# Kernel tuning notes

Measured on AMD Instinct MI355X. Metric: run time of the kernel, lower is better.

The kernel has to match this reference:

```python
import jax, jax.numpy as jnp
import numpy as np
import math

B, T = 32768, 34
VOCAB = 14
SQRT_HD = math.sqrt(3.0)

def _pos_flat_index():
    # flatten (source, index) pairs into indices of a [14,3] table:
    # rows 0-9 = digit spiral enc, row 10 = z10_enc, rows 11-13 = special_enc
    flat = []
    for p in range(34):
        if p < 10:
            flat.append(p)
        elif p == 10:
            flat.append(11 + 0)
        elif p < 21:
            flat.append(p - 11)
        elif p == 21:
            flat.append(11 + 1)
        elif p < 33:
            z = p - 22
            flat.append(z if z < 10 else 10)
        else:
            flat.append(11 + 2)
    return np.array(flat, dtype=np.int32)

POS_FLAT = _pos_flat_index()

def setup_inputs() -> dict:
    key = jax.random.key(0)
    ks = jax.random.split(key, 12)
    r = lambda k, s: jax.random.normal(k, s, dtype=jnp.float32)
    return {
        'idx': jax.random.randint(ks[0], (B, T), 0, VOCAB, dtype=jnp.int64),
        'tok_emb': r(ks[1], (14, 3)),
        'pos_params': r(ks[2], (4,)),
        'z10_enc': r(ks[3], (1, 3)),
        'special_enc': r(ks[4], (3, 3)),
        'wq': r(ks[5], (3, 6)), 'wk': r(ks[6], (3, 6)), 'wv': r(ks[7], (3, 6)),
        'wo': r(ks[8], (6, 6)),
        'ln1_g': jnp.ones(6), 'ln1_b': jnp.zeros(6),
        'ln2_g': jnp.ones(6), 'ln2_b': jnp.zeros(6),
        'lnf_g': jnp.ones(6), 'lnf_b': jnp.zeros(6),
        'ffn_w1': r(ks[9], (6, 2)), 'ffn_b1': jnp.zeros(2),
        'ffn_w2': r(ks[10], (2, 6)), 'ffn_b2': jnp.zeros(6),
        'head_w': r(ks[11], (6, 3)),
    }

def _ln(x, g, b):
    mu = x.mean(-1, keepdims=True)
    var = ((x - mu) ** 2).mean(-1, keepdims=True)
    return (x - mu) * jax.lax.rsqrt(var + 1e-5) * g + b

def _forward(idx, tok_emb, pos_params, z10_enc, special_enc, wq, wk, wv, wo,
             ln1_g, ln1_b, ln2_g, ln2_b, lnf_g, lnf_b,
             ffn_w1, ffn_b1, ffn_w2, ffn_b2, head_w):
    amp, phase, slope, offset = pos_params[0], pos_params[1], pos_params[2], pos_params[3]
    i = jnp.arange(10, dtype=jnp.float32)
    ang = 2.0 * math.pi * i / 10.0 + phase
    digit = jnp.stack([amp * jnp.cos(ang), amp * jnp.sin(ang), slope * i + offset], -1)  # [10,3]
    table = jnp.concatenate([digit, z10_enc, special_enc], 0)  # [14,3]
    Tn = idx.shape[1]
    pos = table[POS_FLAT][:Tn]  # [T,3]
    tok = tok_emb[idx]  # [B,T,3]
    x = jnp.concatenate([tok, jnp.broadcast_to(pos, tok.shape)], -1)  # [B,T,6]
    h = _ln(x, ln1_g, ln1_b)
    h_tok, h_pos = h[..., :3], h[..., 3:]
    Bn = idx.shape[0]
    q = (h_pos @ wq).reshape(Bn, Tn, 2, 3)
    k = (h_pos @ wk).reshape(Bn, Tn, 2, 3)
    v = (h_tok @ wv).reshape(Bn, Tn, 2, 3)
    attn = jnp.einsum('bqhd,bkhd->bhqk', q, k) / SQRT_HD
    mask = jnp.tril(jnp.ones((Tn, Tn), bool))
    attn = jax.nn.softmax(jnp.where(mask, attn, -jnp.inf), axis=-1)
    o = jnp.einsum('bhqk,bkhd->bqhd', attn, v).reshape(Bn, Tn, 6)
    x = x + o @ wo
    h2 = _ln(x, ln2_g, ln2_b)
    x = x + (jax.nn.gelu(h2 @ ffn_w1 + ffn_b1, approximate=False) @ ffn_w2 + ffn_b2)
    x = _ln(x, lnf_g, lnf_b)
    return (x @ head_w) @ tok_emb.T  # [B,T,14]

def reference(idx, tok_emb, pos_params, z10_enc, special_enc, wq, wk, wv, wo,
              ln1_g, ln1_b, ln2_g, ln2_b, lnf_g, lnf_b,
              ffn_w1, ffn_b1, ffn_w2, ffn_b2, head_w):
    return _forward(idx, tok_emb, pos_params, z10_enc, special_enc, wq, wk, wv, wo,
                    ln1_g, ln1_b, ln2_g, ln2_b, lnf_g, lnf_b,
                    ffn_w1, ffn_b1, ffn_w2, ffn_b2, head_w)
```

## Files before the change

kernel.cpp:

```cpp
#include <hip/hip_runtime.h>
#include <math.h>

#define BT    34
#define TPR   17
#define RPB   15
#define BLOCK 256

typedef float v2f __attribute__((ext_vector_type(2)));
typedef float v4f __attribute__((ext_vector_type(4)));

#define QSCALE 0.83294037332470f

#if __has_builtin(__builtin_amdgcn_exp2f)
#define EXP2(x) __builtin_amdgcn_exp2f(x)
#else
#define EXP2(x) exp2f(x)
#endif

__device__ __forceinline__ void ln6p(const v2f* x, const float* g, const float* b, v2f* o) {
  v2f mu = (x[0]+x[1]+x[2]+x[3]+x[4]+x[5]) * (1.0f/6.0f);
  v2f v = (v2f){0.f, 0.f};
  #pragma unroll
  for (int c = 0; c < 6; ++c) { v2f d = x[c]-mu; v += d*d; }
  v2f inv = (v2f){ rsqrtf(v.x*(1.0f/6.0f) + 1e-5f),
                   rsqrtf(v.y*(1.0f/6.0f) + 1e-5f) };
  #pragma unroll
  for (int c = 0; c < 6; ++c) o[c] = (x[c]-mu)*inv*g[c] + b[c];
}

__global__ __launch_bounds__(BLOCK, 5)
void addtrans_kernel(const int* __restrict__ idx,
                     const float* __restrict__ tok_emb,
                     const float* __restrict__ pos_params,
                     const float* __restrict__ z10_enc,
                     const float* __restrict__ special_enc,
                     const float* __restrict__ wq,
                     const float* __restrict__ wk,
                     const float* __restrict__ wv,
                     const float* __restrict__ wo,
                     const float* __restrict__ ln1_g, const float* __restrict__ ln1_b,
                     const float* __restrict__ ln2_g, const float* __restrict__ ln2_b,
                     const float* __restrict__ lnf_g, const float* __restrict__ lnf_b,
                     const float* __restrict__ ffn_w1, const float* __restrict__ ffn_b1,
                     const float* __restrict__ ffn_w2, const float* __restrict__ ffn_b2,
                     const float* __restrict__ head_w,
                     float* __restrict__ out, int B)
{
  __shared__ __align__(16) float s_mem[RPB*BT*14];
  __shared__ int   s_idx[RPB*BT];
  __shared__ float s_te[42];
  __shared__ float s_pos[BT*3];
  __shared__ float s_wq[18], s_wk[18], s_wv[18], s_wo[36], s_hw[18];
  __shared__ float s_g1[6], s_b1[6], s_g2[6], s_b2[6], s_gf[6], s_bf[6];
  __shared__ float s_w1[12], s_w2[12], s_fb1[2], s_fb2[6];

  const int tid = threadIdx.x;
  const int b0  = blockIdx.x * RPB;

  if (tid < 42) s_te[tid] = tok_emb[tid];
  if (tid < 18) { s_wq[tid]=wq[tid]; s_wk[tid]=wk[tid]; s_wv[tid]=wv[tid]; s_hw[tid]=head_w[tid]; }
  if (tid < 36) s_wo[tid] = wo[tid];
  if (tid < 12) { s_w1[tid]=ffn_w1[tid]; s_w2[tid]=ffn_w2[tid]; }
  if (tid < 6)  { s_g1[tid]=ln1_g[tid]; s_b1[tid]=ln1_b[tid];
                  s_g2[tid]=ln2_g[tid]; s_b2[tid]=ln2_b[tid];
                  s_gf[tid]=lnf_g[tid]; s_bf[tid]=lnf_b[tid];
                  s_fb2[tid]=ffn_b2[tid]; }
  if (tid < 2)  s_fb1[tid] = ffn_b1[tid];
  {
    int nr = B - b0; if (nr > RPB) nr = RPB;
    const int tot = nr * BT;
    for (int i = tid; i < tot; i += BLOCK) s_idx[i] = idx[b0*BT + i];
  }
  if (tid < BT) {
    int p = tid, f;
    if (p < 10) f = p;
    else if (p == 10) f = 11;
    else if (p < 21) f = p - 11;
    else if (p == 21) f = 12;
    else if (p < 33) { int z = p - 22; f = (z < 10) ? z : 10; }
    else f = 13;
    float e0, e1, e2;
    if (f < 10) {
      float amp = pos_params[0], ph = pos_params[1], sl = pos_params[2], of = pos_params[3];
      float ang = 0.62831853071795864769f * (float)f + ph;
      e0 = amp * cosf(ang); e1 = amp * sinf(ang); e2 = sl * (float)f + of;
    } else if (f == 10) { e0 = z10_enc[0]; e1 = z10_enc[1]; e2 = z10_enc[2]; }
    else { int u = f - 11; e0 = special_enc[u*3]; e1 = special_enc[u*3+1]; e2 = special_enc[u*3+2]; }
    s_pos[tid*3+0] = e0; s_pos[tid*3+1] = e1; s_pos[tid*3+2] = e2;
  }
  __syncthreads();

  const int row = tid % RPB;
  const int j   = tid / RPB;
  const int b   = b0 + row;
  const bool active = (j < TPR) && (b < B);

  v2f qpA[3], qpB[3];
  v2f x6[6];

  if (active) {
    const int tA = j, tB = j + TPR;
    const int vA = s_idx[row*BT + tA];
    const int vB = s_idx[row*BT + tB];
    #pragma unroll
    for (int c = 0; c < 3; ++c) {
      x6[c]   = (v2f){ s_te[vA*3+c],  s_te[vB*3+c]  };
      x6[3+c] = (v2f){ s_pos[tA*3+c], s_pos[tB*3+c] };
    }
    v2f h[6];
    ln6p(x6, s_g1, s_b1, h);
    v2f q6[6], k6[6], v6[6];
    #pragma unroll
    for (int c = 0; c < 6; ++c) {
      q6[c] = h[3]*s_wq[c] + h[4]*s_wq[6+c] + h[5]*s_wq[12+c];
      k6[c] = h[3]*s_wk[c] + h[4]*s_wk[6+c] + h[5]*s_wk[12+c];
      v6[c] = h[0]*s_wv[c] + h[1]*s_wv[6+c] + h[2]*s_wv[12+c];
    }
    #pragma unroll
    for (int d = 0; d < 3; ++d) {
      qpA[d] = (v2f){ q6[d].x, q6[3+d].x } * QSCALE;
      qpB[d] = (v2f){ q6[d].y, q6[3+d].y } * QSCALE;
    }
    v4f* pA = (v4f*)&s_mem[(tA*RPB + row)*12];
    pA[0] = (v4f){ k6[0].x, k6[3].x, k6[1].x, k6[4].x };
    pA[1] = (v4f){ k6[2].x, k6[5].x, v6[0].x, v6[3].x };
    pA[2] = (v4f){ v6[1].x, v6[4].x, v6[2].x, v6[5].x };
    v4f* pB = (v4f*)&s_mem[(tB*RPB + row)*12];
    pB[0] = (v4f){ k6[0].y, k6[3].y, k6[1].y, k6[4].y };
    pB[1] = (v4f){ k6[2].y, k6[5].y, v6[0].y, v6[3].y };
    pB[2] = (v4f){ v6[1].y, v6[4].y, v6[2].y, v6[5].y };
  }
  __syncthreads();

  v2f l0 = (v2f){0.f,0.f}, l1 = (v2f){0.f,0.f};
  v2f o0[3] = {(v2f){0.f,0.f},(v2f){0.f,0.f},(v2f){0.f,0.f}};
  v2f o1[3] = {(v2f){0.f,0.f},(v2f){0.f,0.f},(v2f){0.f,0.f}};
  if (active) {
    const float* kvbase = s_mem + row*12;
    v4f A  = ((const v4f*)kvbase)[0];
    v4f Bv = ((const v4f*)kvbase)[1];
    v4f C  = ((const v4f*)kvbase)[2];
    for (int k = 0; k <= j; ++k) {
      const v4f Ac = A, Bc = Bv, Cc = C;
      const v4f* nxt = (const v4f*)(kvbase + (k+1)*(RPB*12));
      A = nxt[0]; Bv = nxt[1]; C = nxt[2];
      v2f kA = (v2f){Ac.x, Ac.y}, kB = (v2f){Ac.z, Ac.w}, kC = (v2f){Bc.x, Bc.y};
      v2f vA = (v2f){Bc.z, Bc.w}, vB = (v2f){Cc.x, Cc.y}, vC = (v2f){Cc.z, Cc.w};
      v2f s0 = qpA[0]*kA + qpA[1]*kB + qpA[2]*kC;
      v2f p0 = (v2f){EXP2(s0.x), EXP2(s0.y)};
      l0 += p0; o0[0] += p0*vA; o0[1] += p0*vB; o0[2] += p0*vC;
      v2f s1 = qpB[0]*kA + qpB[1]*kB + qpB[2]*kC;
      v2f p1 = (v2f){EXP2(s1.x), EXP2(s1.y)};
      l1 += p1; o1[0] += p1*vA; o1[1] += p1*vB; o1[2] += p1*vC;
    }
    for (int i = 1; i <= TPR; ++i) {
      const int k = j + i;
      const v4f Ac = A, Bc = Bv, Cc = C;
      const v4f* nxt = (const v4f*)(kvbase + (k+1)*(RPB*12));
      A = nxt[0]; Bv = nxt[1]; C = nxt[2];
      v2f kA = (v2f){Ac.x, Ac.y}, kB = (v2f){Ac.z, Ac.w}, kC = (v2f){Bc.x, Bc.y};
      v2f vA = (v2f){Bc.z, Bc.w}, vB = (v2f){Cc.x, Cc.y}, vC = (v2f){Cc.z, Cc.w};
      v2f s1 = qpB[0]*kA + qpB[1]*kB + qpB[2]*kC;
      v2f p1 = (v2f){EXP2(s1.x), EXP2(s1.y)};
      l1 += p1; o1[0] += p1*vA; o1[1] += p1*vB; o1[2] += p1*vC;
    }
  }
  __syncthreads();

  if (active) {
    const float rA0 = __builtin_amdgcn_rcpf(l0.x);
    const float rA1 = __builtin_amdgcn_rcpf(l0.y);
    const float rB0 = __builtin_amdgcn_rcpf(l1.x);
    const float rB1 = __builtin_amdgcn_rcpf(l1.y);
    v2f a6[6];
    a6[0] = (v2f){ o0[0].x*rA0, o1[0].x*rB0 };
    a6[1] = (v2f){ o0[1].x*rA0, o1[1].x*rB0 };
    a6[2] = (v2f){ o0[2].x*rA0, o1[2].x*rB0 };
    a6[3] = (v2f){ o0[0].y*rA1, o1[0].y*rB1 };
    a6[4] = (v2f){ o0[1].y*rA1, o1[1].y*rB1 };
    a6[5] = (v2f){ o0[2].y*rA1, o1[2].y*rB1 };
    v2f xn[6];
    #pragma unroll
    for (int c = 0; c < 6; ++c) {
      xn[c] = x6[c]
            + a6[0]*s_wo[c]    + a6[1]*s_wo[6+c]  + a6[2]*s_wo[12+c]
            + a6[3]*s_wo[18+c] + a6[4]*s_wo[24+c] + a6[5]*s_wo[30+c];
    }
    v2f h2[6];
    ln6p(xn, s_g2, s_b2, h2);
    v2f a0 = (v2f){s_fb1[0], s_fb1[0]};
    v2f a1 = (v2f){s_fb1[1], s_fb1[1]};
    #pragma unroll
    for (int d = 0; d < 6; ++d) { a0 += h2[d]*s_w1[d*2]; a1 += h2[d]*s_w1[d*2+1]; }
    const float KIS2 = 0.70710678118654752440f;
    v2f g0 = (v2f){ 0.5f*a0.x*(1.0f + erff(a0.x*KIS2)),
                    0.5f*a0.y*(1.0f + erff(a0.y*KIS2)) };
    v2f g1 = (v2f){ 0.5f*a1.x*(1.0f + erff(a1.x*KIS2)),
                    0.5f*a1.y*(1.0f + erff(a1.y*KIS2)) };
    #pragma unroll
    for (int c = 0; c < 6; ++c) xn[c] += g0*s_w2[c] + g1*s_w2[6+c] + s_fb2[c];
    v2f xf[6];
    ln6p(xn, s_gf, s_bf, xf);
    v2f y0 = (v2f){0.f,0.f}, y1 = (v2f){0.f,0.f}, y2 = (v2f){0.f,0.f};
    #pragma unroll
    for (int c = 0; c < 6; ++c) {
      y0 += xf[c]*s_hw[c*3+0]; y1 += xf[c]*s_hw[c*3+1]; y2 += xf[c]*s_hw[c*3+2];
    }
    v2f* lpA = (v2f*)&s_mem[(row*BT + j      )*14];
    v2f* lpB = (v2f*)&s_mem[(row*BT + j + TPR)*14];
    #pragma unroll
    for (int u = 0; u < 7; ++u) {
      const int c0 = 2*u, c1 = 2*u+1;
      v2f lg0 = y0*s_te[c0*3+0] + y1*s_te[c0*3+1] + y2*s_te[c0*3+2];
      v2f lg1 = y0*s_te[c1*3+0] + y1*s_te[c1*3+1] + y2*s_te[c1*3+2];
      lpA[u] = (v2f){ lg0.x, lg1.x };
      lpB[u] = (v2f){ lg0.y, lg1.y };
    }
  }
  __syncthreads();

  {
    int nrows = B - b0; if (nrows > RPB) nrows = RPB;
    if (nrows > 0) {
      const int n4 = nrows * (BT*14/4);
      v4f* dst = reinterpret_cast<v4f*>(out + (size_t)b0 * (BT*14));
      const v4f* src = reinterpret_cast<const v4f*>(s_mem);
      for (int i = tid; i < n4; i += BLOCK)
        __builtin_nontemporal_store(src[i], dst + i);
    }
  }
}

extern "C" void kernel_launch(void* const* d_in, const int* in_sizes, int n_in,
                              void* d_out, int out_size, void* d_ws, size_t ws_size,
                              hipStream_t stream) {
  const int B = in_sizes[0] / BT;
  const int grid = (B + RPB - 1) / RPB;
  addtrans_kernel<<<grid, BLOCK, 0, stream>>>(
      (const int*)d_in[0],   (const float*)d_in[1], (const float*)d_in[2],
      (const float*)d_in[3], (const float*)d_in[4], (const float*)d_in[5],
      (const float*)d_in[6], (const float*)d_in[7], (const float*)d_in[8],
      (const float*)d_in[9], (const float*)d_in[10], (const float*)d_in[11],
      (const float*)d_in[12], (const float*)d_in[13], (const float*)d_in[14],
      (const float*)d_in[15], (const float*)d_in[16], (const float*)d_in[17],
      (const float*)d_in[18], (const float*)d_in[19],
      (float*)d_out, B);
}
```

Measured before the change: 133.6 us.

## Fold LayerNorm affine into weights and write logits directly to global memory

Folds the LayerNorm gamma and beta into the following projection weights and biases, so each LayerNorm only normalises. The shared-memory output staging and its trailing barriers are removed: logits go straight to global memory as 8-byte stores, and idx is read directly from global instead of through shared memory. Shared memory shrinks, so the launch bound is raised to 6 blocks per SIMD, and the second attention loop gets unroll 4. The direct stores are strided per thread rather than coalesced 16-byte nontemporal writes, which risks poorer write efficiency on this output-bound kernel.

Result: slower. 140.5 us (+5.2%).

```diff
diff --git a/kernel.cpp b/kernel.cpp
--- a/kernel.cpp
+++ b/kernel.cpp
@@ -17,7 +17,7 @@
 #define EXP2(x) exp2f(x)
 #endif
 
-__device__ __forceinline__ void ln6p(const v2f* x, const float* g, const float* b, v2f* o) {
+__device__ __forceinline__ void ln6n(const v2f* x, v2f* o) {
   v2f mu = (x[0]+x[1]+x[2]+x[3]+x[4]+x[5]) * (1.0f/6.0f);
   v2f v = (v2f){0.f, 0.f};
   #pragma unroll
@@ -25,10 +25,10 @@
   v2f inv = (v2f){ rsqrtf(v.x*(1.0f/6.0f) + 1e-5f),
                    rsqrtf(v.y*(1.0f/6.0f) + 1e-5f) };
   #pragma unroll
-  for (int c = 0; c < 6; ++c) o[c] = (x[c]-mu)*inv*g[c] + b[c];
+  for (int c = 0; c < 6; ++c) o[c] = (x[c]-mu)*inv;
 }
 
-__global__ __launch_bounds__(BLOCK, 5)
+__global__ __launch_bounds__(BLOCK, 6)
 void addtrans_kernel(const int* __restrict__ idx,
                      const float* __restrict__ tok_emb,
                      const float* __restrict__ pos_params,
@@ -46,30 +46,46 @@
                      const float* __restrict__ head_w,
                      float* __restrict__ out, int B)
 {
-  __shared__ __align__(16) float s_mem[RPB*BT*14];
-  __shared__ int   s_idx[RPB*BT];
+  __shared__ __align__(16) float s_mem[RPB*BT*12 + 180];
   __shared__ float s_te[42];
   __shared__ float s_pos[BT*3];
-  __shared__ float s_wq[18], s_wk[18], s_wv[18], s_wo[36], s_hw[18];
-  __shared__ float s_g1[6], s_b1[6], s_g2[6], s_b2[6], s_gf[6], s_bf[6];
-  __shared__ float s_w1[12], s_w2[12], s_fb1[2], s_fb2[6];
+  __shared__ float s_wqf[18], s_wkf[18], s_wvf[18];
+  __shared__ float s_qb[6], s_kb[6], s_vb[6];
+  __shared__ float s_wo[36];
+  __shared__ float s_w1f[12], s_fb1f[2];
+  __shared__ float s_w2[12], s_fb2[6];
+  __shared__ float s_hwf[18], s_yb[3];
 
   const int tid = threadIdx.x;
   const int b0  = blockIdx.x * RPB;
 
   if (tid < 42) s_te[tid] = tok_emb[tid];
-  if (tid < 18) { s_wq[tid]=wq[tid]; s_wk[tid]=wk[tid]; s_wv[tid]=wv[tid]; s_hw[tid]=head_w[tid]; }
+  if (tid < 18) {
+    const int r = tid / 6;
+    s_wqf[tid] = wq[tid] * ln1_g[3+r];
+    s_wkf[tid] = wk[tid] * ln1_g[3+r];
+    s_wvf[tid] = wv[tid] * ln1_g[r];
+    s_hwf[tid] = head_w[tid] * lnf_g[tid/3];
+  }
   if (tid < 36) s_wo[tid] = wo[tid];
-  if (tid < 12) { s_w1[tid]=ffn_w1[tid]; s_w2[tid]=ffn_w2[tid]; }
-  if (tid < 6)  { s_g1[tid]=ln1_g[tid]; s_b1[tid]=ln1_b[tid];
-                  s_g2[tid]=ln2_g[tid]; s_b2[tid]=ln2_b[tid];
-                  s_gf[tid]=lnf_g[tid]; s_bf[tid]=lnf_b[tid];
-                  s_fb2[tid]=ffn_b2[tid]; }
-  if (tid < 2)  s_fb1[tid] = ffn_b1[tid];
-  {
-    int nr = B - b0; if (nr > RPB) nr = RPB;
-    const int tot = nr * BT;
-    for (int i = tid; i < tot; i += BLOCK) s_idx[i] = idx[b0*BT + i];
+  if (tid < 12) { s_w1f[tid] = ffn_w1[tid] * ln2_g[tid>>1]; s_w2[tid] = ffn_w2[tid]; }
+  if (tid < 6)  {
+    s_qb[tid] = ln1_b[3]*wq[tid] + ln1_b[4]*wq[6+tid] + ln1_b[5]*wq[12+tid];
+    s_kb[tid] = ln1_b[3]*wk[tid] + ln1_b[4]*wk[6+tid] + ln1_b[5]*wk[12+tid];
+    s_vb[tid] = ln1_b[0]*wv[tid] + ln1_b[1]*wv[6+tid] + ln1_b[2]*wv[12+tid];
+    s_fb2[tid] = ffn_b2[tid];
+  }
+  if (tid < 3) {
+    float a = 0.f;
+    #pragma unroll
+    for (int c = 0; c < 6; ++c) a += lnf_b[c]*head_w[c*3+tid];
+    s_yb[tid] = a;
+  }
+  if (tid < 2) {
+    float a = ffn_b1[tid];
+    #pragma unroll
+    for (int d = 0; d < 6; ++d) a += ln2_b[d]*ffn_w1[d*2+tid];
+    s_fb1f[tid] = a;
   }
   if (tid < BT) {
     int p = tid, f;
@@ -100,21 +116,21 @@
 
   if (active) {
     const int tA = j, tB = j + TPR;
-    const int vA = s_idx[row*BT + tA];
-    const int vB = s_idx[row*BT + tB];
+    const int vA = idx[b*BT + tA];
+    const int vB = idx[b*BT + tB];
     #pragma unroll
     for (int c = 0; c < 3; ++c) {
       x6[c]   = (v2f){ s_te[vA*3+c],  s_te[vB*3+c]  };
       x6[3+c] = (v2f){ s_pos[tA*3+c], s_pos[tB*3+c] };
     }
     v2f h[6];
-    ln6p(x6, s_g1, s_b1, h);
+    ln6n(x6, h);
     v2f q6[6], k6[6], v6[6];
     #pragma unroll
     for (int c = 0; c < 6; ++c) {
-      q6[c] = h[3]*s_wq[c] + h[4]*s_wq[6+c] + h[5]*s_wq[12+c];
-      k6[c] = h[3]*s_wk[c] + h[4]*s_wk[6+c] + h[5]*s_wk[12+c];
-      v6[c] = h[0]*s_wv[c] + h[1]*s_wv[6+c] + h[2]*s_wv[12+c];
+      q6[c] = (v2f){s_qb[c], s_qb[c]} + h[3]*s_wqf[c] + h[4]*s_wqf[6+c] + h[5]*s_wqf[12+c];
+      k6[c] = (v2f){s_kb[c], s_kb[c]} + h[3]*s_wkf[c] + h[4]*s_wkf[6+c] + h[5]*s_wkf[12+c];
+      v6[c] = (v2f){s_vb[c], s_vb[c]} + h[0]*s_wvf[c] + h[1]*s_wvf[6+c] + h[2]*s_wvf[12+c];
     }
     #pragma unroll
     for (int d = 0; d < 3; ++d) {
@@ -153,6 +169,7 @@
       v2f p1 = (v2f){EXP2(s1.x), EXP2(s1.y)};
       l1 += p1; o1[0] += p1*vA; o1[1] += p1*vB; o1[2] += p1*vC;
     }
+    #pragma unroll 4
     for (int i = 1; i <= TPR; ++i) {
       const int k = j + i;
       const v4f Ac = A, Bc = Bv, Cc = C;
@@ -165,7 +182,6 @@
       l1 += p1; o1[0] += p1*vA; o1[1] += p1*vB; o1[2] += p1*vC;
     }
   }
-  __syncthreads();
 
   if (active) {
     const float rA0 = __builtin_amdgcn_rcpf(l0.x);
@@ -186,12 +202,12 @@
             + a6[0]*s_wo[c]    + a6[1]*s_wo[6+c]  + a6[2]*s_wo[12+c]
             + a6[3]*s_wo[18+c] + a6[4]*s_wo[24+c] + a6[5]*s_wo[30+c];
     }
-    v2f h2[6];
-    ln6p(xn, s_g2, s_b2, h2);
-    v2f a0 = (v2f){s_fb1[0], s_fb1[0]};
-    v2f a1 = (v2f){s_fb1[1], s_fb1[1]};
-    #pragma unroll
-    for (int d = 0; d < 6; ++d) { a0 += h2[d]*s_w1[d*2]; a1 += h2[d]*s_w1[d*2+1]; }
+    v2f t2[6];
+    ln6n(xn, t2);
+    v2f a0 = (v2f){s_fb1f[0], s_fb1f[0]};
+    v2f a1 = (v2f){s_fb1f[1], s_fb1f[1]};
+    #pragma unroll
+    for (int d = 0; d < 6; ++d) { a0 += t2[d]*s_w1f[d*2]; a1 += t2[d]*s_w1f[d*2+1]; }
     const float KIS2 = 0.70710678118654752440f;
     v2f g0 = (v2f){ 0.5f*a0.x*(1.0f + erff(a0.x*KIS2)),
                     0.5f*a0.y*(1.0f + erff(a0.y*KIS2)) };
@@ -199,34 +215,24 @@
                     0.5f*a1.y*(1.0f + erff(a1.y*KIS2)) };
     #pragma unroll
     for (int c = 0; c < 6; ++c) xn[c] += g0*s_w2[c] + g1*s_w2[6+c] + s_fb2[c];
-    v2f xf[6];
-    ln6p(xn, s_gf, s_bf, xf);
-    v2f y0 = (v2f){0.f,0.f}, y1 = (v2f){0.f,0.f}, y2 = (v2f){0.f,0.f};
+    v2f tf[6];
+    ln6n(xn, tf);
+    v2f y0 = (v2f){s_yb[0], s_yb[0]};
+    v2f y1 = (v2f){s_yb[1], s_yb[1]};
+    v2f y2 = (v2f){s_yb[2], s_yb[2]};
     #pragma unroll
     for (int c = 0; c < 6; ++c) {
-      y0 += xf[c]*s_hw[c*3+0]; y1 += xf[c]*s_hw[c*3+1]; y2 += xf[c]*s_hw[c*3+2];
-    }
-    v2f* lpA = (v2f*)&s_mem[(row*BT + j      )*14];
-    v2f* lpB = (v2f*)&s_mem[(row*BT + j + TPR)*14];
+      y0 += tf[c]*s_hwf[c*3+0]; y1 += tf[c]*s_hwf[c*3+1]; y2 += tf[c]*s_hwf[c*3+2];
+    }
+    float* oA = out + ((size_t)b * BT + j) * 14;
+    float* oB = oA + TPR * 14;
     #pragma unroll
     for (int u = 0; u < 7; ++u) {
       const int c0 = 2*u, c1 = 2*u+1;
       v2f lg0 = y0*s_te[c0*3+0] + y1*s_te[c0*3+1] + y2*s_te[c0*3+2];
       v2f lg1 = y0*s_te[c1*3+0] + y1*s_te[c1*3+1] + y2*s_te[c1*3+2];
-      lpA[u] = (v2f){ lg0.x, lg1.x };
-      lpB[u] = (v2f){ lg0.y, lg1.y };
-    }
-  }
-  __syncthreads();
-
-  {
-    int nrows = B - b0; if (nrows > RPB) nrows = RPB;
-    if (nrows > 0) {
-      const int n4 = nrows * (BT*14/4);
-      v4f* dst = reinterpret_cast<v4f*>(out + (size_t)b0 * (BT*14));
-      const v4f* src = reinterpret_cast<const v4f*>(s_mem);
-      for (int i = tid; i < n4; i += BLOCK)
-        __builtin_nontemporal_store(src[i], dst + i);
+      *reinterpret_cast<v2f*>(oA + 2*u) = (v2f){ lg0.x, lg1.x };
+      *reinterpret_cast<v2f*>(oB + 2*u) = (v2f){ lg0.y, lg1.y };
     }
   }
 }
```
